# Kernel optimization log

Hardware: AMD Instinct MI355X
Metric: run time of the kernel (lower is better)

Reference implementation:

```python
import jax, jax.numpy as jnp
import numpy as np

B, T, C, H = 256, 256, 384, 6
HS = C // H        # 64 head size
P = int(C * 0.8)   # 307 pca_dim
EPS = 1e-6


def _rmsnorm(x, scale):
    rms = jnp.sqrt(jnp.mean(x * x, axis=-1, keepdims=True) + EPS)
    return x / rms * scale


def _orth(W):
    # torch.svd returns V (not V^T); u @ v.t() == u @ vt
    u, _, vt = jnp.linalg.svd(W, full_matrices=False)
    return u @ vt


def setup_inputs() -> dict:
    key = jax.random.key(0)
    ks = jax.random.split(key, 16)
    s = 0.02
    inp = {
        'x': jax.random.normal(ks[0], (B, T, C), jnp.float32),
        'Wq': jax.random.normal(ks[1], (H, C, HS), jnp.float32) * s,
        'Wk': jax.random.normal(ks[2], (H, C, HS), jnp.float32) * s,
        'Wv': jax.random.normal(ks[3], (H, C, HS), jnp.float32) * s,
        'Wp': jax.random.normal(ks[4], (H * HS, C), jnp.float32) * s,
        'bp': jnp.zeros((C,), jnp.float32),
        'scale1': jnp.ones((C,), jnp.float32),
        'scale2': jnp.ones((C,), jnp.float32),
        'W1': jax.random.normal(ks[5], (C, P), jnp.float32) * s,
        'b1': jnp.zeros((P,), jnp.float32),
        'W2': jax.random.normal(ks[6], (P, C), jnp.float32) * s,
        'b2': jnp.zeros((C,), jnp.float32),
        'Wo_in': jax.random.normal(ks[7], (C, C), jnp.float32),
        'Wo_out': jax.random.normal(ks[8], (C, C), jnp.float32),
    }
    return inp


def reference(x, Wq, Wk, Wv, Wp, bp, scale1, scale2, W1, b1, W2, b2, Wo_in, Wo_out):
    # ln1
    h = _rmsnorm(x, scale1)                                   # [B,T,C]
    # multi-head causal self-attention (heads batched via einsum)
    q = jnp.einsum('btc,hcd->bhtd', h, Wq)                    # [B,H,T,HS]
    k = jnp.einsum('btc,hcd->bhtd', h, Wk)
    v = jnp.einsum('btc,hcd->bhtd', h, Wv)
    wei = jnp.einsum('bhtd,bhsd->bhts', q, k) * (HS ** -0.5)  # [B,H,T,T]
    causal = jnp.tril(jnp.ones((T, T), bool))
    wei = jnp.where(causal, wei, -jnp.inf)
    wei = jax.nn.softmax(wei, axis=-1)
    attn = jnp.einsum('bhts,bhsd->bhtd', wei, v)              # [B,H,T,HS]
    attn = attn.transpose(0, 2, 1, 3).reshape(B, T, H * HS)   # concat heads
    h = attn @ Wp + bp + h                                    # residual on ln1 output
    # ln2
    h = _rmsnorm(h, scale2)
    # input orthogonal transform
    h = h @ _orth(Wo_in)
    # PCA feed-forward (dropout = identity in eval)
    h = jax.nn.relu(h @ W1 + b1)
    h = h @ W2 + b2
    # output orthogonal transform + residual on ff output
    out = h @ _orth(Wo_out) + h
    return out
```

## Files before the change

### kernel.cpp

```cpp
#include <hip/hip_runtime.h>

typedef unsigned short u16;
typedef unsigned int   u32;
typedef short s16x8 __attribute__((ext_vector_type(8)));
typedef float f32x4 __attribute__((ext_vector_type(4)));

static __device__ __forceinline__ float bf2f(u16 v){ return __uint_as_float(((u32)v)<<16); }
static __device__ __forceinline__ u16 f2bf(float f){
  u32 u = __float_as_uint(f);
  u32 r = (u + 0x7fffu + ((u>>16)&1u)) >> 16;
  return (u16)r;
}
static __device__ __forceinline__ float cvt(float v){ return v; }
static __device__ __forceinline__ float cvt(u16 v){ return bf2f(v); }
static __device__ __forceinline__ void stv(float* p, float v){ *p = v; }
static __device__ __forceinline__ void stv(u16* p, float v){ *p = f2bf(v); }

static __device__ __forceinline__ void ld2(const float* p, float& a, float& b){
  float2 t = *(const float2*)p; a=t.x; b=t.y;
}
static __device__ __forceinline__ void ld2(const u16* p, float& a, float& b){
  u32 t = *(const u32*)p; a = __uint_as_float(t<<16); b = __uint_as_float(t & 0xffff0000u);
}
static __device__ __forceinline__ void st2(float* p, float a, float b){
  float2 t; t.x=a; t.y=b; *(float2*)p = t;
}
static __device__ __forceinline__ void st2(u16* p, float a, float b){
  *(u32*)p = ((u32)f2bf(a)) | (((u32)f2bf(b))<<16);
}

static __device__ __forceinline__ void gload16(const u16* g, u16* l){
  __builtin_amdgcn_global_load_lds(
      (const __attribute__((address_space(1))) u32*)(const void*)g,
      (__attribute__((address_space(3))) u32*)(void*)l, 16, 0, 0);
}

template<typename TI, typename TO>
__global__ __launch_bounds__(256) void rms_k(const TI* __restrict__ X,
                                             const float* __restrict__ scale,
                                             TO* __restrict__ O)
{
  int row = blockIdx.x*4 + (threadIdx.x>>6);
  int lane = threadIdx.x&63;
  const TI* xr = X + (size_t)row*384;
  float v[6]; float ss = 0.f;
#pragma unroll
  for(int i=0;i<3;i++){
    ld2(xr + 2*lane + 128*i, v[2*i], v[2*i+1]);
    ss += v[2*i]*v[2*i] + v[2*i+1]*v[2*i+1];
  }
#pragma unroll
  for(int off=32; off>0; off>>=1) ss += __shfl_down(ss, off, 64);
  ss = __shfl(ss, 0, 64);
  float r = rsqrtf(ss*(1.0f/384.0f)+1e-6f);
  TO* orow = O + (size_t)row*384;
#pragma unroll
  for(int i=0;i<3;i++){
    int c = 2*lane + 128*i;
    st2(orow + c, v[2*i]*r*scale[c], v[2*i+1]*r*scale[c+1]);
  }
}

__global__ __launch_bounds__(256) void tcast_k(const float* __restrict__ In, long isz,
                                               u16* __restrict__ Out, long osz,
                                               int Rr, int Cc, int ldo)
{
  __shared__ float t[32][33];
  const int z = blockIdx.z;
  const float* I = In + (long)z*isz;
  u16* Oz = Out + (long)z*osz;
  const int r0 = blockIdx.x*32, c0 = blockIdx.y*32;
  const int tx = threadIdx.x&31, ty = threadIdx.x>>5;
#pragma unroll
  for(int rr=ty; rr<32; rr+=8){
    int r = r0+rr, c = c0+tx;
    t[rr][tx] = (r<Rr && c<Cc) ? I[(size_t)r*Cc + c] : 0.f;
  }
  __syncthreads();
#pragma unroll
  for(int cc=ty; cc<32; cc+=8){
    int c = c0+cc, r = r0+tx;
    if(c<Cc && r<ldo) Oz[(size_t)c*ldo + r] = f2bf(t[tx][cc]);
  }
}

template<int NF, typename TC, typename TR>
__global__ __launch_bounds__(256,3) void mgemm2_k(
    const u16* __restrict__ A, int lda,
    const u16* __restrict__ Bt, int ldb,
    TC* __restrict__ C, long cs_hi, int cs_lo, int csz,
    const TR* __restrict__ R,
    const float* __restrict__ bias,
    int N, int Nstore, int K, float beta, int relu, int nby)
{
  constexpr int BN = NF*32;
  __shared__ __align__(16) u16 As[128*64];
  __shared__ __align__(16) u16 Bs[BN*64];
  const int d = blockIdx.x;
  const int xcd = d&7, slot = d>>3;
  const int bm = xcd*64 + slot/nby;
  const int bn = slot - (slot/nby)*nby;
  const int m0 = bm*128, n0 = bn*BN;
  const int tid = threadIdx.x;
  const int w = tid>>6, lane = tid&63;
  const int g4 = lane>>4, l16 = lane&15;
  const int wr = w>>1, wc = w&1;
  const int srow = lane>>3;
  const int sc8  = ((lane&7) ^ srow) * 8;
  const u16* aSrc[4];
#pragma unroll
  for(int i=0;i<4;i++)
    aSrc[i] = A + (size_t)(m0 + 8*(w+4*i) + srow)*lda + sc8;
  const u16* bSrc[NF];
#pragma unroll
  for(int i=0;i<NF;i++)
    bSrc[i] = Bt + (size_t)(n0 + 8*(w+4*i) + srow)*ldb + sc8;

  f32x4 fz = {0.f,0.f,0.f,0.f};
  f32x4 acc[4][NF];
#pragma unroll
  for(int i=0;i<4;i++)
#pragma unroll
    for(int j=0;j<NF;j++) acc[i][j]=fz;

  const int sxor = l16&7;
  for(int k0=0;k0<K;k0+=64){
#pragma unroll
    for(int i=0;i<4;i++)  gload16(aSrc[i] + k0, &As[(w+4*i)*512]);
#pragma unroll
    for(int i=0;i<NF;i++) gload16(bSrc[i] + k0, &Bs[(w+4*i)*512]);
    __syncthreads();
#pragma unroll
    for(int ks=0; ks<2; ++ks){
      s16x8 av[4];
#pragma unroll
      for(int mf=0;mf<4;mf++){
        int Rr_ = wr*64 + mf*16 + l16;
        av[mf] = *(const s16x8*)&As[Rr_*64 + 8*((ks*4+g4) ^ sxor)];
      }
      s16x8 bv[NF];
#pragma unroll
      for(int nf=0;nf<NF;nf++){
        int Rn = wc*(NF*16) + nf*16 + l16;
        bv[nf] = *(const s16x8*)&Bs[Rn*64 + 8*((ks*4+g4) ^ sxor)];
      }
#pragma unroll
      for(int mf=0;mf<4;mf++)
#pragma unroll
        for(int nf=0;nf<NF;nf++)
          acc[mf][nf] = __builtin_amdgcn_mfma_f32_16x16x32_bf16(av[mf], bv[nf], acc[mf][nf], 0,0,0);
    }
    __syncthreads();
  }
#pragma unroll
  for(int mf=0;mf<4;mf++)
#pragma unroll
    for(int i=0;i<4;i++){
      int m = m0 + wr*64 + mf*16 + g4*4 + i;
      long rowoff = (long)(m>>8)*cs_hi + (long)(m&255)*cs_lo;
#pragma unroll
      for(int nf=0;nf<NF;nf++){
        int gn = n0 + wc*(NF*16) + nf*16 + l16;
        if(gn < Nstore){
          long addr = rowoff + (long)(gn>>6)*csz + (gn&63);
          float v = 0.f;
          if(gn < N){
            v = acc[mf][nf][i];
            if(R)    v += beta*cvt(R[addr]);
            if(bias) v += bias[gn];
            if(relu) v  = fmaxf(v, 0.f);
          }
          stv(C + addr, v);
        }
      }
    }
}

__global__ __launch_bounds__(256,2) void mattn_k(const u16* __restrict__ QKV,
                                                 u16* __restrict__ O)
{
  __shared__ __align__(16) u16 Ks[64*64];
  __shared__ __align__(16) u16 Vts[64*64];
  __shared__ __align__(16) u16 Ps[4*4096];
  const int bh = blockIdx.x;
  const int b = bh/6, h = bh - b*6;
  const u16* Qb = QKV + (size_t)bh*49152;
  const u16* Kb = Qb + 16384;
  const u16* Vb = Qb + 32768;
  const int tid = threadIdx.x;
  const int w = tid>>6, lane = tid&63;
  const int g4 = lane>>4, l16 = lane&15;
  char* PB = (char*)&Ps[w*4096];
  const int swz = (l16&7)<<4;

  s16x8 qf[4][2];
#pragma unroll
  for(int mi=0;mi<4;mi++)
#pragma unroll
    for(int ks=0;ks<2;ks++)
      qf[mi][ks] = *(const s16x8*)(Qb + (size_t)(w*64 + mi*16 + l16)*64 + ks*32 + g4*8);

  f32x4 fzv = {0.f,0.f,0.f,0.f};
  f32x4 o[4][4];
#pragma unroll
  for(int mf=0;mf<4;mf++)
#pragma unroll
    for(int df=0;df<4;df++) o[mf][df]=fzv;
  float mrun[4], lrun[4];
#pragma unroll
  for(int mi=0;mi<4;mi++){ mrun[mi]=-1e30f; lrun[mi]=0.f; }

  for(int st=0; st<4; ++st){
    if(st) __syncthreads();
#pragma unroll
    for(int it=0; it<2; ++it){
      int c = tid + 256*it;
      int s = c>>3, d0 = (c&7)*8;
      uint4 ld = *(const uint4*)(Kb + (size_t)(st*64+s)*64 + d0);
      int byte = s*128 + d0*2; byte ^= (s&7)<<4;
      *(uint4*)((char*)Ks + byte) = ld;
    }
#pragma unroll
    for(int it=0; it<2; ++it){
      int c = tid + 256*it;
      int s = c&63, d0 = (c>>6)*8;
      uint4 ld = *(const uint4*)(Vb + (size_t)(st*64+s)*64 + d0);
#pragma unroll
      for(int jj=0; jj<4; ++jj){
        u32 ww = (jj==0)?ld.x:(jj==1)?ld.y:(jj==2)?ld.z:ld.w;
        int d = d0 + 2*jj;
        int byte0 = d*128 + s*2;     byte0 ^= (d&7)<<4;
        int byte1 = (d+1)*128 + s*2; byte1 ^= ((d+1)&7)<<4;
        *(u16*)((char*)Vts + byte0) = (u16)(ww & 0xffffu);
        *(u16*)((char*)Vts + byte1) = (u16)(ww >> 16);
      }
    }
    __syncthreads();
    if(w < st) continue;

    f32x4 sc[4][4];
#pragma unroll
    for(int sf=0; sf<4; ++sf){
      int row = sf*16 + l16;
      s16x8 kf0 = *(const s16x8*)((char*)Ks + ((row*128 + g4*16) ^ swz));
      s16x8 kf1 = *(const s16x8*)((char*)Ks + ((row*128 + 64 + g4*16) ^ swz));
#pragma unroll
      for(int mi=0; mi<4; ++mi){
        f32x4 t = __builtin_amdgcn_mfma_f32_16x16x32_bf16(kf0, qf[mi][0], fzv, 0,0,0);
        sc[sf][mi] = __builtin_amdgcn_mfma_f32_16x16x32_bf16(kf1, qf[mi][1], t, 0,0,0);
      }
    }
    float alpha[4];
#pragma unroll
    for(int mi=0; mi<4; ++mi){
      int mloc = mi*16 + l16;
      float rmax = -3.0e38f;
#pragma unroll
      for(int sf=0; sf<4; ++sf)
#pragma unroll
        for(int i=0;i<4;i++){
          float vv = sc[sf][mi][i]*0.125f;
          if(st==w && (sf*16 + g4*4 + i) > mloc) vv = -1e30f;
          sc[sf][mi][i] = vv;
          rmax = fmaxf(rmax, vv);
        }
      rmax = fmaxf(rmax, __shfl_xor(rmax, 16, 64));
      rmax = fmaxf(rmax, __shfl_xor(rmax, 32, 64));
      float mnew = fmaxf(mrun[mi], rmax);
      float al = __expf(mrun[mi] - mnew);
      mrun[mi] = mnew;
      float ls = 0.f;
#pragma unroll
      for(int sf=0; sf<4; ++sf){
        float p0 = __expf(sc[sf][mi][0]-mnew);
        float p1 = __expf(sc[sf][mi][1]-mnew);
        float p2 = __expf(sc[sf][mi][2]-mnew);
        float p3 = __expf(sc[sf][mi][3]-mnew);
        ls += p0+p1+p2+p3;
        ushort4 pk; pk.x=f2bf(p0); pk.y=f2bf(p1); pk.z=f2bf(p2); pk.w=f2bf(p3);
        int byte = mloc*128 + sf*32 + g4*8; byte ^= (l16&7)<<4;
        *(ushort4*)(PB + byte) = pk;
      }
      ls += __shfl_xor(ls, 16, 64);
      ls += __shfl_xor(ls, 32, 64);
      lrun[mi] = lrun[mi]*al + ls;
      alpha[mi] = al;
    }
#pragma unroll
    for(int mf=0; mf<4; ++mf)
#pragma unroll
      for(int i=0;i<4;i++){
        float at = __shfl(alpha[mf], g4*4 + i, 64);
#pragma unroll
        for(int df=0; df<4; ++df) o[mf][df][i] *= at;
      }
    s16x8 vbf[4][2];
#pragma unroll
    for(int df=0; df<4; ++df){
      int row = df*16 + l16;
      vbf[df][0] = *(const s16x8*)((char*)Vts + ((row*128 + g4*16) ^ swz));
      vbf[df][1] = *(const s16x8*)((char*)Vts + ((row*128 + 64 + g4*16) ^ swz));
    }
#pragma unroll
    for(int mf=0; mf<4; ++mf){
      int row = mf*16 + l16;
      s16x8 pa0 = *(const s16x8*)(PB + ((row*128 + g4*16) ^ swz));
      s16x8 pa1 = *(const s16x8*)(PB + ((row*128 + 64 + g4*16) ^ swz));
#pragma unroll
      for(int df=0; df<4; ++df){
        f32x4 t = __builtin_amdgcn_mfma_f32_16x16x32_bf16(pa0, vbf[df][0], o[mf][df], 0,0,0);
        o[mf][df] = __builtin_amdgcn_mfma_f32_16x16x32_bf16(pa1, vbf[df][1], t, 0,0,0);
      }
    }
  }
#pragma unroll
  for(int mf=0; mf<4; ++mf)
#pragma unroll
    for(int i=0;i<4;i++){
      float lt = __shfl(lrun[mf], g4*4 + i, 64);
      float rl = 1.f/lt;
      u16* orow = O + ((size_t)(b*256 + w*64 + mf*16 + g4*4 + i))*384 + h*64;
#pragma unroll
      for(int df=0; df<4; ++df)
        orow[df*16 + l16] = f2bf(o[mf][df][i]*rl);
    }
}

__global__ __launch_bounds__(256) void fpart_k(const float* __restrict__ W0,
                                               const float* __restrict__ W1,
                                               float* __restrict__ part)
{
  int b = blockIdx.x; int z = b/24, seg = b - z*24;
  const float* W = (z ? W1 : W0) + seg*6144;
  int tid = threadIdx.x;
  float s = 0.f;
  for(int i=tid;i<6144;i+=256){ float v=W[i]; s+=v*v; }
#pragma unroll
  for(int off=32; off>0; off>>=1) s += __shfl_down(s, off, 64);
  __shared__ float red[4];
  if((tid&63)==0) red[tid>>6]=s;
  __syncthreads();
  if(tid==0) part[b] = red[0]+red[1]+red[2]+red[3];
}

__global__ __launch_bounds__(64) void fcomb_k(const float* __restrict__ part,
                                              float* __restrict__ invb)
{
  int lane = threadIdx.x;
  float v = 0.f;
  if(lane < 24) v = part[lane];
  else if(lane >= 32 && lane < 56) v = part[lane - 8];
#pragma unroll
  for(int off=1; off<32; off<<=1) v += __shfl_xor(v, off, 64);
  if(lane==0)  invb[0] = rsqrtf(v);
  if(lane==32) invb[1] = rsqrtf(v);
}

__global__ __launch_bounds__(256) void nsinit_k(const float* __restrict__ W0,
                                                const float* __restrict__ W1,
                                                const float* __restrict__ invb,
                                                u16* __restrict__ XB)
{
  int b = blockIdx.x; int z = b/24, p = b - z*24, cp0 = p*16;
  const float* W = z ? W1 : W0;
  float inv = invb[z];
  u16* base = XB + (size_t)z*589824;
  u16* xh = base;            u16* xl = base + 147456;
  u16* th = base + 294912;   u16* tl = base + 442368;
  int tid = threadIdx.x;
  for(int idx=tid; idx<6144; idx+=256){
    int r = idx>>4, j = idx&15;
    float v = W[r*384 + cp0 + j]*inv;
    u16 hh = f2bf(v);
    xh[p*6144 + idx] = hh;
    xl[p*6144 + idx] = f2bf(v - bf2f(hh));
  }
  for(int idx=tid; idx<6144; idx+=256){
    int j = idx/384, r = idx - j*384;
    float v = W[(cp0+j)*384 + r]*inv;
    u16 hh = f2bf(v);
    th[p*6144 + r*16 + j] = hh;
    tl[p*6144 + r*16 + j] = f2bf(v - bf2f(hh));
  }
}

static __device__ __forceinline__ void ns_mm(
    const u16* __restrict__ Agh, const u16* __restrict__ Agl,
    u16* AhL, u16* AlL, const u16* BThL, const u16* BTlL,
    int tid, f32x4 acc[4])
{
  const int w = tid>>6, lane = tid&63, g4 = lane>>4, l16 = lane&15;
  const int o0 = (tid>>1)*24 + (tid&1)*8;
  const int o1 = o0 + 4608;
  const s16x8 z8 = {0,0,0,0,0,0,0,0};
  f32x4 fz = {0.f,0.f,0.f,0.f};
#pragma unroll
  for(int i=0;i<4;i++) acc[i]=fz;
  {
    uint4 h0 = *(const uint4*)(Agh + tid*8);
    uint4 h1 = *(const uint4*)(Agh + (384+tid)*8);
    uint4 l0 = *(const uint4*)(Agl + tid*8);
    uint4 l1 = *(const uint4*)(Agl + (384+tid)*8);
    *(uint4*)&AhL[o0] = h0; *(uint4*)&AhL[o1] = h1;
    *(uint4*)&AlL[o0] = l0; *(uint4*)&AlL[o1] = l1;
  }
  __syncthreads();
  for(int c=0;c<24;c++){
    uint4 nh0, nh1, nl0, nl1;
    if(c<23){
      const u16* ph = Agh + (c+1)*6144;
      const u16* pl = Agl + (c+1)*6144;
      nh0 = *(const uint4*)(ph + tid*8);
      nh1 = *(const uint4*)(ph + (384+tid)*8);
      nl0 = *(const uint4*)(pl + tid*8);
      nl1 = *(const uint4*)(pl + (384+tid)*8);
    }
    s16x8 bh = z8, bl = z8;
    if(g4<2){
      bh = *(const s16x8*)&BThL[l16*392 + c*16 + g4*8];
      bl = *(const s16x8*)&BTlL[l16*392 + c*16 + g4*8];
    }
#pragma unroll
    for(int tt=0;tt<4;tt++){
      int rb = 64*w + 16*tt + l16;
      s16x8 ah = z8, al = z8;
      if(g4<2){
        ah = *(const s16x8*)&AhL[rb*24 + g4*8];
        al = *(const s16x8*)&AlL[rb*24 + g4*8];
      }
      acc[tt] = __builtin_amdgcn_mfma_f32_16x16x32_bf16(ah, bh, acc[tt], 0,0,0);
      acc[tt] = __builtin_amdgcn_mfma_f32_16x16x32_bf16(ah, bl, acc[tt], 0,0,0);
      acc[tt] = __builtin_amdgcn_mfma_f32_16x16x32_bf16(al, bh, acc[tt], 0,0,0);
    }
    __syncthreads();
    if(c<23){
      *(uint4*)&AhL[o0] = nh0; *(uint4*)&AhL[o1] = nh1;
      *(uint4*)&AlL[o0] = nl0; *(uint4*)&AlL[o1] = nl1;
      __syncthreads();
    }
  }
}

__global__ __launch_bounds__(384) void nsit_k(u16* __restrict__ XB,
                                              u16* __restrict__ QT,
                                              int it, int niter, int nq)
{
  __shared__ __align__(16) u16 AhL[384*24];
  __shared__ __align__(16) u16 AlL[384*24];
  __shared__ __align__(16) u16 BTh[16*392];
  __shared__ __align__(16) u16 BTl[16*392];
  const int blk = blockIdx.x;
  const int z = blk/24, p = blk - z*24, cp0 = p*16;
  const int tid = threadIdx.x;
  const int w = tid>>6, lane = tid&63, g4 = lane>>4, l16 = lane&15;
  const int rs = it&1, ws2 = rs^1;
  const u16* bin  = XB + (size_t)rs*1179648  + (size_t)z*589824;
  u16*       bout = XB + (size_t)ws2*1179648 + (size_t)z*589824;
  const u16* Xh  = bin;            const u16* Xl  = bin + 147456;
  const u16* Th  = bin + 294912;   const u16* Tl  = bin + 442368;

  {
    const u16* sh = Xh + p*6144;
    const u16* sl = Xl + p*6144;
    for(int i=tid; i<768; i+=384){
      int k = i>>1, n0 = (i&1)*8;
      uint4 vh = *(const uint4*)(sh + i*8);
      uint4 vl = *(const uint4*)(sl + i*8);
#pragma unroll
      for(int j=0;j<8;j++){
        BTh[(n0+j)*392 + k] = ((u16*)&vh)[j];
        BTl[(n0+j)*392 + k] = ((u16*)&vl)[j];
      }
    }
  }
  __syncthreads();

  const bool quint = (it < nq);
  f32x4 acc[4], gsv[4];

  ns_mm(Th, Tl, AhL, AlL, BTh, BTl, tid, acc);
  if(quint){
#pragma unroll
    for(int tt=0;tt<4;tt++){
      gsv[tt] = acc[tt];
      int m0 = 64*w + 16*tt + g4*4;
      ushort4 h4, l4;
#pragma unroll
      for(int i=0;i<4;i++){
        float v = acc[tt][i];
        u16 hh = f2bf(v);
        ((u16*)&h4)[i]=hh; ((u16*)&l4)[i]=f2bf(v - bf2f(hh));
      }
      *(ushort4*)&BTh[l16*392 + m0] = h4;
      *(ushort4*)&BTl[l16*392 + m0] = l4;
    }
    __syncthreads();
    ns_mm(Xh, Xl, AhL, AlL, BTh, BTl, tid, acc);
#pragma unroll
    for(int tt=0;tt<4;tt++){
      int m0 = 64*w + 16*tt + g4*4;
      ushort4 h4, l4;
#pragma unroll
      for(int i=0;i<4;i++){
        float v = acc[tt][i];
        u16 hh = f2bf(v);
        ((u16*)&h4)[i]=hh; ((u16*)&l4)[i]=f2bf(v - bf2f(hh));
      }
      *(ushort4*)&BTh[l16*392 + m0] = h4;
      *(ushort4*)&BTl[l16*392 + m0] = l4;
    }
    __syncthreads();
    ns_mm(Th, Tl, AhL, AlL, BTh, BTl, tid, acc);
    __syncthreads();
#pragma unroll
    for(int tt=0;tt<4;tt++){
      int m0 = 64*w + 16*tt + g4*4;
      ushort4 h4, l4;
#pragma unroll
      for(int i=0;i<4;i++){
        float v = fmaf(2.0315f, acc[tt][i], -4.7750f*(gsv[tt][i]))
                + ((m0+i)==(cp0+l16) ? 3.4445f : 0.f);
        u16 hh = f2bf(v);
        ((u16*)&h4)[i]=hh; ((u16*)&l4)[i]=f2bf(v - bf2f(hh));
      }
      *(ushort4*)&BTh[l16*392 + m0] = h4;
      *(ushort4*)&BTl[l16*392 + m0] = l4;
    }
    __syncthreads();
  } else {
#pragma unroll
    for(int tt=0;tt<4;tt++){
      int m0 = 64*w + 16*tt + g4*4;
      ushort4 h4, l4;
#pragma unroll
      for(int i=0;i<4;i++){
        float v = -0.5f*acc[tt][i] + ((m0+i)==(cp0+l16) ? 1.5f : 0.f);
        u16 hh = f2bf(v);
        ((u16*)&h4)[i]=hh; ((u16*)&l4)[i]=f2bf(v - bf2f(hh));
      }
      *(ushort4*)&BTh[l16*392 + m0] = h4;
      *(ushort4*)&BTl[l16*392 + m0] = l4;
    }
    __syncthreads();
  }
  ns_mm(Xh, Xl, AhL, AlL, BTh, BTl, tid, acc);

  if(it == niter-1){
    u16* q = QT + (size_t)z*147456 + (size_t)(cp0+l16)*384;
#pragma unroll
    for(int tt=0;tt<4;tt++){
      int m0 = 64*w + 16*tt + g4*4;
      ushort4 h4;
#pragma unroll
      for(int i=0;i<4;i++) ((u16*)&h4)[i] = f2bf(acc[tt][i]);
      *(ushort4*)&q[m0] = h4;
    }
  } else {
    u16* oXh = bout + p*6144;            u16* oXl = bout + 147456 + p*6144;
    u16* oTh = bout + 294912;            u16* oTl = bout + 442368;
#pragma unroll
    for(int tt=0;tt<4;tt++){
      int m0 = 64*w + 16*tt + g4*4;
      ushort4 h4, l4;
#pragma unroll
      for(int i=0;i<4;i++){
        float v = acc[tt][i];
        u16 hh = f2bf(v);
        ((u16*)&h4)[i]=hh; ((u16*)&l4)[i]=f2bf(v - bf2f(hh));
        oXh[(m0+i)*16 + l16] = hh;
        oXl[(m0+i)*16 + l16] = ((u16*)&l4)[i];
      }
      size_t to = (size_t)(4*w+tt)*6144 + (size_t)(cp0+l16)*16 + g4*4;
      *(ushort4*)&oTh[to] = h4;
      *(ushort4*)&oTl[to] = l4;
    }
  }
}

extern "C" void kernel_launch(void* const* d_in, const int* in_sizes, int n_in,
                              void* d_out, int out_size, void* d_ws, size_t ws_size,
                              hipStream_t stream)
{
  const float* x      = (const float*)d_in[0];
  const float* Wq     = (const float*)d_in[1];
  const float* Wk     = (const float*)d_in[2];
  const float* Wv     = (const float*)d_in[3];
  const float* Wp     = (const float*)d_in[4];
  const float* bp     = (const float*)d_in[5];
  const float* scale1 = (const float*)d_in[6];
  const float* scale2 = (const float*)d_in[7];
  const float* W1     = (const float*)d_in[8];
  const float* b1     = (const float*)d_in[9];
  const float* W2     = (const float*)d_in[10];
  const float* b2     = (const float*)d_in[11];
  const float* Wo_in  = (const float*)d_in[12];
  const float* Wo_out = (const float*)d_in[13];

  char* ws = (char*)d_ws;
  u16* XB   = (u16*)(ws + 0);
  u16* Wqkv = (u16*)(ws + 4719104L);
  u16* WpT  = (u16*)(ws + 5603840L);
  u16* W1T  = (u16*)(ws + 5898752L);
  u16* W2T  = (u16*)(ws + 6134528L);
  u16* QT   = (u16*)(ws + 6380288L);
  float* part = (float*)(ws + 6970112L);
  float* invb = (float*)(ws + 6970496L);
  u16* h1b  = (u16*)(ws + 8388608L);
  u16* qkvb = (u16*)(ws + 58720256L);
  u16* atb  = (u16*)(ws + 209715200L);
  u16* h2b = qkvb;
  u16* h3b = qkvb + 25165824L;
  u16* h4b = qkvb + 50331648L;
  u16* h5b = atb;
  u16* h6b = h1b;

  tcast_k<<<dim3(12, 2,6),256,0,stream>>>(Wq,24576L, Wqkv,        73728L, 384, 64,384);
  tcast_k<<<dim3(12, 2,6),256,0,stream>>>(Wk,24576L, Wqkv+24576L, 73728L, 384, 64,384);
  tcast_k<<<dim3(12, 2,6),256,0,stream>>>(Wv,24576L, Wqkv+49152L, 73728L, 384, 64,384);
  tcast_k<<<dim3(12,12,1),256,0,stream>>>(Wp,0L,     WpT,0L,     384,384,384);
  tcast_k<<<dim3(12,10,1),256,0,stream>>>(W1,0L,     W1T,0L,     384,307,384);
  tcast_k<<<dim3(10,12,1),256,0,stream>>>(W2,0L,     W2T,0L,     307,384,320);

  const int NITER = 15, NQ = 10;
  fpart_k<<<48,256,0,stream>>>(Wo_in, Wo_out, part);
  fcomb_k<<<1,64,0,stream>>>(part, invb);
  nsinit_k<<<48,256,0,stream>>>(Wo_in, Wo_out, invb, XB);
  for(int it=0; it<NITER; ++it)
    nsit_k<<<48,384,0,stream>>>(XB, QT, it, NITER, NQ);

  rms_k<float,u16><<<16384,256,0,stream>>>(x, scale1, h1b);
  mgemm2_k<6,u16,float><<<3072,256,0,stream>>>(
      h1b,384,  Wqkv,384,
      qkvb, 294912L,64,16384,
      (const float*)nullptr, nullptr,
      1152,1152,384, 0.f,0, 6);
  mattn_k<<<1536,256,0,stream>>>(qkvb, atb);
  mgemm2_k<6,u16,u16><<<1024,256,0,stream>>>(
      atb,384,  WpT,384,
      h2b, 98304L,384,64,
      h1b, bp,
      384,384,384, 1.f,0, 2);
  rms_k<u16,u16><<<16384,256,0,stream>>>(h2b, scale2, h3b);
  mgemm2_k<6,u16,float><<<1024,256,0,stream>>>(
      h3b,384,  QT,384,
      h4b, 98304L,384,64,
      (const float*)nullptr, nullptr,
      384,384,384, 0.f,0, 2);
  mgemm2_k<5,u16,float><<<1024,256,0,stream>>>(
      h4b,384,  W1T,384,
      h5b, 81920L,320,64,
      (const float*)nullptr, b1,
      307,320,384, 0.f,1, 2);
  mgemm2_k<6,u16,float><<<1024,256,0,stream>>>(
      h5b,320,  W2T,320,
      h6b, 98304L,384,64,
      (const float*)nullptr, b2,
      384,384,320, 0.f,0, 2);
  mgemm2_k<6,float,u16><<<1024,256,0,stream>>>(
      h6b,384,  QT+147456,384,
      (float*)d_out, 98304L,384,64,
      h6b, nullptr,
      384,384,384, 1.f,0, 2);

  (void)in_sizes; (void)n_in; (void)ws_size; (void)out_size;
}
```

Measured before the change: 1.595 ms.

## Shrink GEMM N-tiles, raise occupancy, read Newton-Schulz A operands directly from global

All GEMM launches now use a 64-wide N tile (NF=2) instead of 192/160, with three times as many blocks, and the launch-bounds occupancy hint rises from 3 to 4 blocks per CU. The Newton-Schulz iteration kernel drops its shared-memory staging of the A operand and its per-chunk barriers, loading MFMA fragments straight from global memory. The aim is more parallelism and latency hiding in the GEMMs and less synchronisation in the orthogonalisation loop. The trade-off is less B-tile reuse per block, more redundant A-tile loads, and uncoalesced or uncached global reads in the NS matmul.

```diff
diff --git a/kernel.cpp b/kernel.cpp
--- a/kernel.cpp
+++ b/kernel.cpp
@@ -85,7 +85,7 @@
 }
 
 template<int NF, typename TC, typename TR>
-__global__ __launch_bounds__(256,3) void mgemm2_k(
+__global__ __launch_bounds__(256,4) void mgemm2_k(
     const u16* __restrict__ A, int lda,
     const u16* __restrict__ Bt, int ldb,
     TC* __restrict__ C, long cs_hi, int cs_lo, int csz,
@@ -384,60 +384,36 @@
   }
 }
 
-static __device__ __forceinline__ void ns_mm(
+static __device__ __forceinline__ void ns_mm2(
     const u16* __restrict__ Agh, const u16* __restrict__ Agl,
-    u16* AhL, u16* AlL, const u16* BThL, const u16* BTlL,
+    const u16* BThL, const u16* BTlL,
     int tid, f32x4 acc[4])
 {
   const int w = tid>>6, lane = tid&63, g4 = lane>>4, l16 = lane&15;
-  const int o0 = (tid>>1)*24 + (tid&1)*8;
-  const int o1 = o0 + 4608;
   const s16x8 z8 = {0,0,0,0,0,0,0,0};
   f32x4 fz = {0.f,0.f,0.f,0.f};
 #pragma unroll
   for(int i=0;i<4;i++) acc[i]=fz;
-  {
-    uint4 h0 = *(const uint4*)(Agh + tid*8);
-    uint4 h1 = *(const uint4*)(Agh + (384+tid)*8);
-    uint4 l0 = *(const uint4*)(Agl + tid*8);
-    uint4 l1 = *(const uint4*)(Agl + (384+tid)*8);
-    *(uint4*)&AhL[o0] = h0; *(uint4*)&AhL[o1] = h1;
-    *(uint4*)&AlL[o0] = l0; *(uint4*)&AlL[o1] = l1;
-  }
-  __syncthreads();
+  const bool act = (g4<2);
+#pragma unroll 4
   for(int c=0;c<24;c++){
-    uint4 nh0, nh1, nl0, nl1;
-    if(c<23){
-      const u16* ph = Agh + (c+1)*6144;
-      const u16* pl = Agl + (c+1)*6144;
-      nh0 = *(const uint4*)(ph + tid*8);
-      nh1 = *(const uint4*)(ph + (384+tid)*8);
-      nl0 = *(const uint4*)(pl + tid*8);
-      nl1 = *(const uint4*)(pl + (384+tid)*8);
-    }
     s16x8 bh = z8, bl = z8;
-    if(g4<2){
+    if(act){
       bh = *(const s16x8*)&BThL[l16*392 + c*16 + g4*8];
       bl = *(const s16x8*)&BTlL[l16*392 + c*16 + g4*8];
     }
 #pragma unroll
     for(int tt=0;tt<4;tt++){
-      int rb = 64*w + 16*tt + l16;
+      const int rb = 64*w + 16*tt + l16;
       s16x8 ah = z8, al = z8;
-      if(g4<2){
-        ah = *(const s16x8*)&AhL[rb*24 + g4*8];
-        al = *(const s16x8*)&AlL[rb*24 + g4*8];
+      if(act){
+        ah = *(const s16x8*)&Agh[c*6144 + rb*16 + g4*8];
+        al = *(const s16x8*)&Agl[c*6144 + rb*16 + g4*8];
       }
       acc[tt] = __builtin_amdgcn_mfma_f32_16x16x32_bf16(ah, bh, acc[tt], 0,0,0);
       acc[tt] = __builtin_amdgcn_mfma_f32_16x16x32_bf16(ah, bl, acc[tt], 0,0,0);
       acc[tt] = __builtin_amdgcn_mfma_f32_16x16x32_bf16(al, bh, acc[tt], 0,0,0);
     }
-    __syncthreads();
-    if(c<23){
-      *(uint4*)&AhL[o0] = nh0; *(uint4*)&AhL[o1] = nh1;
-      *(uint4*)&AlL[o0] = nl0; *(uint4*)&AlL[o1] = nl1;
-      __syncthreads();
-    }
   }
 }
 
@@ -445,17 +421,15 @@
                                               u16* __restrict__ QT,
                                               int it, int niter, int nq)
 {
-  __shared__ __align__(16) u16 AhL[384*24];
-  __shared__ __align__(16) u16 AlL[384*24];
   __shared__ __align__(16) u16 BTh[16*392];
   __shared__ __align__(16) u16 BTl[16*392];
   const int blk = blockIdx.x;
   const int z = blk/24, p = blk - z*24, cp0 = p*16;
   const int tid = threadIdx.x;
   const int w = tid>>6, lane = tid&63, g4 = lane>>4, l16 = lane&15;
-  const int rs = it&1, ws2 = rs^1;
-  const u16* bin  = XB + (size_t)rs*1179648  + (size_t)z*589824;
-  u16*       bout = XB + (size_t)ws2*1179648 + (size_t)z*589824;
+  const int rs = it&1;
+  const u16* bin  = XB + (size_t)rs*1179648     + (size_t)z*589824;
+  u16*       bout = XB + (size_t)(rs^1)*1179648 + (size_t)z*589824;
   const u16* Xh  = bin;            const u16* Xl  = bin + 147456;
   const u16* Th  = bin + 294912;   const u16* Tl  = bin + 442368;
 
@@ -478,7 +452,8 @@
   const bool quint = (it < nq);
   f32x4 acc[4], gsv[4];
 
-  ns_mm(Th, Tl, AhL, AlL, BTh, BTl, tid, acc);
+  ns_mm2(Th, Tl, BTh, BTl, tid, acc);
+  __syncthreads();
   if(quint){
 #pragma unroll
     for(int tt=0;tt<4;tt++){
@@ -495,7 +470,8 @@
       *(ushort4*)&BTl[l16*392 + m0] = l4;
     }
     __syncthreads();
-    ns_mm(Xh, Xl, AhL, AlL, BTh, BTl, tid, acc);
+    ns_mm2(Xh, Xl, BTh, BTl, tid, acc);
+    __syncthreads();
 #pragma unroll
     for(int tt=0;tt<4;tt++){
       int m0 = 64*w + 16*tt + g4*4;
@@ -510,7 +486,7 @@
       *(ushort4*)&BTl[l16*392 + m0] = l4;
     }
     __syncthreads();
-    ns_mm(Th, Tl, AhL, AlL, BTh, BTl, tid, acc);
+    ns_mm2(Th, Tl, BTh, BTl, tid, acc);
     __syncthreads();
 #pragma unroll
     for(int tt=0;tt<4;tt++){
@@ -543,7 +519,7 @@
     }
     __syncthreads();
   }
-  ns_mm(Xh, Xl, AhL, AlL, BTh, BTl, tid, acc);
+  ns_mm2(Xh, Xl, BTh, BTl, tid, acc);
 
   if(it == niter-1){
     u16* q = QT + (size_t)z*147456 + (size_t)(cp0+l16)*384;
@@ -629,38 +605,38 @@
     nsit_k<<<48,384,0,stream>>>(XB, QT, it, NITER, NQ);
 
   rms_k<float,u16><<<16384,256,0,stream>>>(x, scale1, h1b);
-  mgemm2_k<6,u16,float><<<3072,256,0,stream>>>(
+  mgemm2_k<2,u16,float><<<9216,256,0,stream>>>(
       h1b,384,  Wqkv,384,
       qkvb, 294912L,64,16384,
       (const float*)nullptr, nullptr,
-      1152,1152,384, 0.f,0, 6);
+      1152,1152,384, 0.f,0, 18);
   mattn_k<<<1536,256,0,stream>>>(qkvb, atb);
-  mgemm2_k<6,u16,u16><<<1024,256,0,stream>>>(
+  mgemm2_k<2,u16,u16><<<3072,256,0,stream>>>(
       atb,384,  WpT,384,
       h2b, 98304L,384,64,
       h1b, bp,
-      384,384,384, 1.f,0, 2);
+      384,384,384, 1.f,0, 6);
   rms_k<u16,u16><<<16384,256,0,stream>>>(h2b, scale2, h3b);
-  mgemm2_k<6,u16,float><<<1024,256,0,stream>>>(
+  mgemm2_k<2,u16,float><<<3072,256,0,stream>>>(
       h3b,384,  QT,384,
       h4b, 98304L,384,64,
       (const float*)nullptr, nullptr,
-      384,384,384, 0.f,0, 2);
-  mgemm2_k<5,u16,float><<<1024,256,0,stream>>>(
+      384,384,384, 0.f,0, 6);
+  mgemm2_k<2,u16,float><<<2560,256,0,stream>>>(
       h4b,384,  W1T,384,
       h5b, 81920L,320,64,
       (const float*)nullptr, b1,
-      307,320,384, 0.f,1, 2);
-  mgemm2_k<6,u16,float><<<1024,256,0,stream>>>(
+      307,320,384, 0.f,1, 5);
+  mgemm2_k<2,u16,float><<<3072,256,0,stream>>>(
       h5b,320,  W2T,320,
       h6b, 98304L,384,64,
       (const float*)nullptr, b2,
-      384,384,320, 0.f,0, 2);
-  mgemm2_k<6,float,u16><<<1024,256,0,stream>>>(
+      384,384,320, 0.f,0, 6);
+  mgemm2_k<2,float,u16><<<3072,256,0,stream>>>(
       h6b,384,  QT+147456,384,
       (float*)d_out, 98304L,384,64,
       h6b, nullptr,
-      384,384,384, 1.f,0, 2);
+      384,384,384, 1.f,0, 6);
 
   (void)in_sizes; (void)n_in; (void)ws_size; (void)out_size;
 }
```

Result: slower. 1.927 ms (+20.8%).
